# Kernel tuning notes

Hardware: AMD Instinct MI355X
Metric: run time of the kernel (lower is better)

The kernel has to match this reference:

```python
import jax, jax.numpy as jnp
import numpy as np

N_NODES = 50000
N_EDGES = 1600000
IN_FEAT = 256
HID = IN_FEAT // 2  # 128
OUT_FEAT = 256


def setup_inputs() -> dict:
    key = jax.random.key(0)
    ks = jax.random.split(key, 10)
    x = jax.random.normal(ks[0], (N_NODES, IN_FEAT), dtype=jnp.float32)
    w = jax.random.uniform(ks[1], (N_EDGES, 1), dtype=jnp.float32)
    src = jax.random.randint(ks[2], (N_EDGES,), 0, N_NODES, dtype=jnp.int32)
    dst = jax.random.randint(ks[3], (N_EDGES,), 0, N_NODES, dtype=jnp.int32)
    s = 1.0 / np.sqrt(IN_FEAT)
    W_node = jax.random.uniform(ks[4], (IN_FEAT, HID), jnp.float32, -s, s)
    b_node = jax.random.uniform(ks[5], (HID,), jnp.float32, -s, s)
    W_edge = jax.random.uniform(ks[6], (IN_FEAT, HID), jnp.float32, -s, s)
    b_edge = jax.random.uniform(ks[7], (HID,), jnp.float32, -s, s)
    s2 = 1.0 / np.sqrt(HID)
    W_mlp = jax.random.uniform(ks[8], (HID, OUT_FEAT), jnp.float32, -s2, s2)
    b_mlp = jax.random.uniform(ks[9], (OUT_FEAT,), jnp.float32, -s2, s2)
    return {"x": x, "w": w, "src": src, "dst": dst,
            "W_node": W_node, "b_node": b_node,
            "W_edge": W_edge, "b_edge": b_edge,
            "W_mlp": W_mlp, "b_mlp": b_mlp}


def reference(x, w, src, dst, W_node, b_node, W_edge, b_edge, W_mlp, b_mlp):
    # message[v] = sum_{(u->v) in E} x[u] * w_e   (src_mul_edge + sum)
    message = jax.ops.segment_sum(x[src] * w, dst, num_segments=x.shape[0])  # [N, in_feat]
    h = (x @ W_node + b_node) + (message @ W_edge + b_edge)  # [N, in_feat//2]
    # NOTE: original uses nn.LeakyReLU(True) -> negative_slope=1.0 (identity);
    # replicated faithfully.
    h = jax.nn.leaky_relu(h, negative_slope=1.0)
    return h @ W_mlp + b_mlp  # [N, out_feat]
```

## Files before the change

kernel.cpp:

```cpp
#include <hip/hip_runtime.h>


constexpr int N_NODES  = 50000;
constexpr int N_EDGES  = 1600000;
constexpr int IN_FEAT  = 256;
constexpr int HID      = 128;
constexpr int OUT_FEAT = 256;

constexpr int BIN_SZ   = 32;
constexpr int N_BINS   = (N_NODES + BIN_SZ - 1) / BIN_SZ;
constexpr int CAPBIN   = 1536;
constexpr int EPB      = 4096;
constexpr int N_CBLK   = (N_EDGES + EPB - 1) / EPB;
constexpr int GRID_M   = (N_NODES + 127) / 128;
constexpr int N_G1BLK  = GRID_M * 2;

typedef __attribute__((ext_vector_type(8))) short bf16x8;
typedef __attribute__((ext_vector_type(8))) unsigned short u16x8;
typedef __attribute__((ext_vector_type(4))) float f32x4;

static __device__ __forceinline__ unsigned short f2bf(float f) {
    unsigned u = __builtin_bit_cast(unsigned, f);
    u += 0x7FFF + ((u >> 16) & 1);
    return (unsigned short)(u >> 16);
}
static __device__ __forceinline__ float bflo(unsigned u) {
    return __builtin_bit_cast(float, u << 16);
}
static __device__ __forceinline__ float bfhi(unsigned u) {
    return __builtin_bit_cast(float, u & 0xFFFF0000u);
}

__global__ __launch_bounds__(256) void k0_convert(
    const float* __restrict__ Wn, const float* __restrict__ We,
    const float* __restrict__ Wm,
    unsigned short* __restrict__ Wcat_t, unsigned short* __restrict__ Wmt)
{
    int n = blockIdx.x;
    int k = threadIdx.x;
    float v = (n < HID) ? Wn[(size_t)k * HID + n] : We[(size_t)k * HID + (n - HID)];
    Wcat_t[(size_t)n * IN_FEAT + k] = f2bf(v);
    if (k < HID) Wmt[(size_t)n * HID + k] = f2bf(Wm[(size_t)k * OUT_FEAT + n]);
}

union SharedU {
    struct {
        int  hist[N_BINS];
        int  gbase[N_BINS];
        int  wsum[8];
        int  stot;
        int2 sorted[EPB];
    } bc;
    struct {
        unsigned short As[128][64];
        unsigned short Bs[128][64];
    } g1;
};

__global__ __launch_bounds__(512, 4) void fuse1(
    const int* __restrict__ src, const int* __restrict__ dst,
    const float* __restrict__ w, int* __restrict__ cursor,
    int2* __restrict__ entries,
    const float* __restrict__ x, const unsigned short* __restrict__ Wcat_t,
    const float* __restrict__ bn, const float* __restrict__ be,
    float* __restrict__ h0, unsigned short* __restrict__ ybf)
{
    __shared__ SharedU sh;
    const int t = threadIdx.x;
    const int wave = t >> 6, lane = t & 63;

    if (blockIdx.x < N_CBLK) {
        const int e0 = blockIdx.x * EPB;

        for (int i = t; i < N_BINS; i += 512) sh.bc.hist[i] = 0;
        __syncthreads();

        int meta[8], wb[8], rk[8], bin[8];
        #pragma unroll
        for (int k = 0; k < 8; ++k) {
            int e = e0 + t + k * 512;
            bin[k] = -1;
            if (e < N_EDGES) {
                int d = dst[e];
                int b = d >> 5;
                bin[k]  = b;
                meta[k] = src[e] | ((d & 31) << 16) | (b << 21);
                wb[k]   = __float_as_int(w[e]);
                rk[k]   = atomicAdd(&sh.bc.hist[b], 1);
            }
        }
        __syncthreads();

        const int b4 = t * 4;
        int c0 = 0, c1 = 0, c2 = 0, c3 = 0;
        if (b4 + 0 < N_BINS) c0 = sh.bc.hist[b4 + 0];
        if (b4 + 1 < N_BINS) c1 = sh.bc.hist[b4 + 1];
        if (b4 + 2 < N_BINS) c2 = sh.bc.hist[b4 + 2];
        if (b4 + 3 < N_BINS) c3 = sh.bc.hist[b4 + 3];
        const int s = c0 + c1 + c2 + c3;
        int pre = s;
        #pragma unroll
        for (int off = 1; off < 64; off <<= 1) {
            int o = __shfl_up(pre, off, 64);
            if (lane >= off) pre += o;
        }
        if (lane == 63) sh.bc.wsum[wave] = pre;
        __syncthreads();
        if (t == 0) {
            int r = 0;
            #pragma unroll
            for (int q = 0; q < 8; ++q) { int v = sh.bc.wsum[q]; sh.bc.wsum[q] = r; r += v; }
            sh.bc.stot = r;
        }
        __syncthreads();
        const int tb = sh.bc.wsum[wave] + pre - s;

        if (b4 + 0 < N_BINS) {
            sh.bc.hist[b4 + 0]  = tb;
            sh.bc.gbase[b4 + 0] = c0 ? atomicAdd(&cursor[b4 + 0], c0) : 0;
        }
        if (b4 + 1 < N_BINS) {
            sh.bc.hist[b4 + 1]  = tb + c0;
            sh.bc.gbase[b4 + 1] = c1 ? atomicAdd(&cursor[b4 + 1], c1) : 0;
        }
        if (b4 + 2 < N_BINS) {
            sh.bc.hist[b4 + 2]  = tb + c0 + c1;
            sh.bc.gbase[b4 + 2] = c2 ? atomicAdd(&cursor[b4 + 2], c2) : 0;
        }
        if (b4 + 3 < N_BINS) {
            sh.bc.hist[b4 + 3]  = tb + c0 + c1 + c2;
            sh.bc.gbase[b4 + 3] = c3 ? atomicAdd(&cursor[b4 + 3], c3) : 0;
        }
        __syncthreads();

        #pragma unroll
        for (int k = 0; k < 8; ++k)
            if (bin[k] >= 0)
                sh.bc.sorted[sh.bc.hist[bin[k]] + rk[k]] = make_int2(meta[k], wb[k]);
        __syncthreads();

        const int tot = sh.bc.stot;
        #pragma unroll
        for (int k = 0; k < 8; ++k) {
            int i = t + k * 512;
            if (i < tot) {
                int2 q = sh.bc.sorted[i];
                int b = ((unsigned)q.x) >> 21;
                int r = i - sh.bc.hist[b];
                int g = sh.bc.gbase[b] + r;
                if (g < CAPBIN)
                    entries[(size_t)b * CAPBIN + g] = make_int2(q.x & 0x1FFFFF, q.y);
            }
        }
    } else {
        const int bid2 = blockIdx.x - N_CBLK;
        const int m0 = (bid2 >> 1) * 128;
        const int nhalf = bid2 & 1;
        const int n0r = nhalf * 128;

        const int wm = wave >> 2, wn = wave & 3;
        const int la = lane & 15, kq = lane >> 4;
        const int srow = t >> 3, sc8 = t & 7;

        f32x4 acc[4][2];
        const f32x4 zero = {0.f, 0.f, 0.f, 0.f};
        #pragma unroll
        for (int i = 0; i < 4; ++i)
            #pragma unroll
            for (int j = 0; j < 2; ++j) acc[i][j] = zero;

        const float4* xg = (const float4*)x;

        for (int kt = 0; kt < 4; ++kt) {
            if (kt) __syncthreads();
            #pragma unroll
            for (int i = 0; i < 2; ++i) {
                int row = srow + i * 64;
                int node = m0 + row;
                float4 v0 = make_float4(0.f, 0.f, 0.f, 0.f), v1 = v0;
                if (node < N_NODES) {
                    v0 = xg[(size_t)node * 64 + kt * 16 + sc8 * 2];
                    v1 = xg[(size_t)node * 64 + kt * 16 + sc8 * 2 + 1];
                }
                u16x8 b;
                b[0] = f2bf(v0.x); b[1] = f2bf(v0.y); b[2] = f2bf(v0.z); b[3] = f2bf(v0.w);
                b[4] = f2bf(v1.x); b[5] = f2bf(v1.y); b[6] = f2bf(v1.z); b[7] = f2bf(v1.w);
                *(u16x8*)&sh.g1.As[row][(sc8 ^ (row & 7)) * 8] = b;
            }
            #pragma unroll
            for (int i = 0; i < 2; ++i) {
                int row = srow + i * 64;
                float4 v = *(const float4*)(
                    Wcat_t + (size_t)(n0r + row) * IN_FEAT + kt * 64 + sc8 * 8);
                *(float4*)&sh.g1.Bs[row][(sc8 ^ (row & 7)) * 8] = v;
            }
            __syncthreads();

            #pragma unroll
            for (int ks = 0; ks < 2; ++ks) {
                bf16x8 a[4], b[2];
                #pragma unroll
                for (int i = 0; i < 4; ++i) {
                    int row = wm * 64 + i * 16 + la;
                    a[i] = *(const bf16x8*)&sh.g1.As[row][((ks * 4 + kq) ^ (row & 7)) * 8];
                }
                #pragma unroll
                for (int j = 0; j < 2; ++j) {
                    int row = wn * 32 + j * 16 + la;
                    b[j] = *(const bf16x8*)&sh.g1.Bs[row][((ks * 4 + kq) ^ (row & 7)) * 8];
                }
                #pragma unroll
                for (int i = 0; i < 4; ++i)
                    #pragma unroll
                    for (int j = 0; j < 2; ++j)
                        acc[i][j] = __builtin_amdgcn_mfma_f32_16x16x32_bf16(
                            a[i], b[j], acc[i][j], 0, 0, 0);
            }
        }

        float bias[2];
        if (nhalf == 0) {
            #pragma unroll
            for (int j = 0; j < 2; ++j) {
                int n = wn * 32 + j * 16 + la;
                bias[j] = bn[n] + be[n];
            }
        }
        #pragma unroll
        for (int i = 0; i < 4; ++i) {
            int mbase = m0 + wm * 64 + i * 16 + kq * 4;
            #pragma unroll
            for (int j = 0; j < 2; ++j) {
                int n = wn * 32 + j * 16 + la;
                #pragma unroll
                for (int r = 0; r < 4; ++r) {
                    int m = mbase + r;
                    if (m < N_NODES) {
                        if (nhalf == 0)
                            h0[(size_t)m * HID + n] = acc[i][j][r] + bias[j];
                        else
                            ybf[(size_t)m * HID + n] = f2bf(acc[i][j][r]);
                    }
                }
            }
        }
    }
}

__global__ __launch_bounds__(512) void gatherB(
    const unsigned short* __restrict__ ybf, const float* __restrict__ h0,
    const int* __restrict__ cursor, const int2* __restrict__ entries,
    unsigned short* __restrict__ hbf)
{
    __shared__ int2 sorted[CAPBIN];
    __shared__ int  cnt32[BIN_SZ];
    __shared__ int  offs32[BIN_SZ];

    const int t = threadIdx.x;
    const int bin = blockIdx.x;
    const int node0 = bin * BIN_SZ;
    const int wave = t >> 6, lane = t & 63;

    const int tot = min(cursor[bin], CAPBIN);
    if (t < BIN_SZ) cnt32[t] = 0;
    __syncthreads();

    int2 held[3];
    int  hrank[3], hdloc[3];
    #pragma unroll
    for (int k = 0; k < 3; ++k) {
        hdloc[k] = -1;
        int g = t + k * 512;
        if (g < tot) {
            int2 ep = entries[(size_t)bin * CAPBIN + g];
            int dloc = ep.x >> 16;
            held[k]  = make_int2(ep.x & 0xFFFF, ep.y);
            hdloc[k] = dloc;
            hrank[k] = atomicAdd(&cnt32[dloc], 1);
        }
    }
    __syncthreads();

    if (wave == 0) {
        int v = (lane < BIN_SZ) ? cnt32[lane] : 0;
        int sum = v;
        #pragma unroll
        for (int off = 1; off < BIN_SZ; off <<= 1) {
            int o = __shfl_up(sum, off, 64);
            if (lane >= off) sum += o;
        }
        if (lane < BIN_SZ) offs32[lane] = sum - v;
    }
    __syncthreads();

    #pragma unroll
    for (int k = 0; k < 3; ++k)
        if (hdloc[k] >= 0)
            sorted[offs32[hdloc[k]] + hrank[k]] = held[k];
    __syncthreads();

    #pragma unroll
    for (int n4 = 0; n4 < 4; ++n4) {
        const int nl = wave * 4 + n4;
        const int node = node0 + nl;
        const int beg = offs32[nl];
        const int c = cnt32[nl];
        float a0 = 0.f, a1 = 0.f;
        int j = 0;
        for (; j + 4 <= c; j += 4) {
            int2 q0 = sorted[beg + j];
            int2 q1 = sorted[beg + j + 1];
            int2 q2 = sorted[beg + j + 2];
            int2 q3 = sorted[beg + j + 3];
            unsigned u0 = *(const unsigned*)&ybf[(size_t)q0.x * HID + 2 * lane];
            unsigned u1 = *(const unsigned*)&ybf[(size_t)q1.x * HID + 2 * lane];
            unsigned u2 = *(const unsigned*)&ybf[(size_t)q2.x * HID + 2 * lane];
            unsigned u3 = *(const unsigned*)&ybf[(size_t)q3.x * HID + 2 * lane];
            float w0 = __int_as_float(q0.y), w1 = __int_as_float(q1.y);
            float w2 = __int_as_float(q2.y), w3 = __int_as_float(q3.y);
            a0 += w0 * bflo(u0); a1 += w0 * bfhi(u0);
            a0 += w1 * bflo(u1); a1 += w1 * bfhi(u1);
            a0 += w2 * bflo(u2); a1 += w2 * bfhi(u2);
            a0 += w3 * bflo(u3); a1 += w3 * bfhi(u3);
        }
        for (; j < c; ++j) {
            int2 q = sorted[beg + j];
            unsigned u = *(const unsigned*)&ybf[(size_t)q.x * HID + 2 * lane];
            float wq = __int_as_float(q.y);
            a0 += wq * bflo(u); a1 += wq * bfhi(u);
        }
        if (node < N_NODES) {
            float2 hv = *(const float2*)&h0[(size_t)node * HID + 2 * lane];
            unsigned r = ((unsigned)f2bf(hv.y + a1) << 16)
                       | (unsigned)f2bf(hv.x + a0);
            *(unsigned*)&hbf[(size_t)node * HID + 2 * lane] = r;
        }
    }
}

__global__ __launch_bounds__(256, 4) void gemm2(
    const unsigned short* __restrict__ hbf, const unsigned short* __restrict__ Wmt,
    const float* __restrict__ bm, float* __restrict__ out)
{
    __shared__ unsigned short As[128][64];
    __shared__ unsigned short Bs[128][64];
    const int t = threadIdx.x;
    const int m0 = blockIdx.x * 128;
    const int n0 = blockIdx.y * 128;

    const int wave = t >> 6, lane = t & 63;
    const int wm = wave & 1, wn = wave >> 1;
    const int la = lane & 15, kq = lane >> 4;
    const int srow = t >> 3, sc8 = t & 7;

    f32x4 acc[4][4];
    const f32x4 zero = {0.f, 0.f, 0.f, 0.f};
    #pragma unroll
    for (int i = 0; i < 4; ++i)
        #pragma unroll
        for (int j = 0; j < 4; ++j) acc[i][j] = zero;

    for (int kt = 0; kt < 2; ++kt) {
        if (kt) __syncthreads();
        #pragma unroll
        for (int i = 0; i < 4; ++i) {
            int row = srow + i * 32;
            int node = m0 + row;
            if (node >= N_NODES) node = N_NODES - 1;
            float4 va = *(const float4*)(hbf + (size_t)node * HID + kt * 64 + sc8 * 8);
            float4 vb = *(const float4*)(Wmt + (size_t)(n0 + row) * HID + kt * 64 + sc8 * 8);
            *(float4*)&As[row][(sc8 ^ (row & 7)) * 8] = va;
            *(float4*)&Bs[row][(sc8 ^ (row & 7)) * 8] = vb;
        }
        __syncthreads();

        #pragma unroll
        for (int ks = 0; ks < 2; ++ks) {
            bf16x8 a[4], b[4];
            #pragma unroll
            for (int i = 0; i < 4; ++i) {
                int row = wm * 64 + i * 16 + la;
                a[i] = *(const bf16x8*)&As[row][((ks * 4 + kq) ^ (row & 7)) * 8];
            }
            #pragma unroll
            for (int j = 0; j < 4; ++j) {
                int row = wn * 64 + j * 16 + la;
                b[j] = *(const bf16x8*)&Bs[row][((ks * 4 + kq) ^ (row & 7)) * 8];
            }
            #pragma unroll
            for (int i = 0; i < 4; ++i)
                #pragma unroll
                for (int j = 0; j < 4; ++j)
                    acc[i][j] = __builtin_amdgcn_mfma_f32_16x16x32_bf16(
                        a[i], b[j], acc[i][j], 0, 0, 0);
        }
    }

    #pragma unroll
    for (int i = 0; i < 4; ++i) {
        int mbase = m0 + wm * 64 + i * 16 + kq * 4;
        #pragma unroll
        for (int j = 0; j < 4; ++j) {
            int n = n0 + wn * 64 + j * 16 + la;
            float b = bm[n];
            #pragma unroll
            for (int r = 0; r < 4; ++r) {
                int m = mbase + r;
                if (m < N_NODES)
                    out[(size_t)m * OUT_FEAT + n] = acc[i][j][r] + b;
            }
        }
    }
}

extern "C" void kernel_launch(void* const* d_in, const int* in_sizes, int n_in,
                              void* d_out, int out_size, void* d_ws, size_t ws_size,
                              hipStream_t stream) {
    const float* x   = (const float*)d_in[0];
    const float* w   = (const float*)d_in[1];
    const int*   src = (const int*)d_in[2];
    const int*   dst = (const int*)d_in[3];
    const float* Wn  = (const float*)d_in[4];
    const float* bn  = (const float*)d_in[5];
    const float* We  = (const float*)d_in[6];
    const float* be  = (const float*)d_in[7];
    const float* Wm  = (const float*)d_in[8];
    const float* bm  = (const float*)d_in[9];
    float* out = (float*)d_out;

    char* p = (char*)d_ws;
    float*          h0      = (float*)p;          p += (size_t)N_NODES * HID * 4;
    unsigned short* ybf     = (unsigned short*)p; p += (size_t)N_NODES * HID * 2;
    unsigned short* hbf     = (unsigned short*)p; p += (size_t)N_NODES * HID * 2;
    int2*           entries = (int2*)p;           p += (size_t)N_BINS * CAPBIN * 8;
    unsigned short* Wcat_t  = (unsigned short*)p; p += (size_t)256 * IN_FEAT * 2;
    unsigned short* Wmt     = (unsigned short*)p; p += (size_t)OUT_FEAT * HID * 2;
    int*            cursor  = (int*)p;            p += (size_t)N_BINS * 4;

    dim3 blk(256);

    hipMemsetAsync(cursor, 0, (size_t)N_BINS * 4, stream);
    k0_convert<<<256, blk, 0, stream>>>(Wn, We, Wm, Wcat_t, Wmt);
    fuse1<<<N_CBLK + N_G1BLK, dim3(512), 0, stream>>>(
        src, dst, w, cursor, entries, x, Wcat_t, bn, be, h0, ybf);
    gatherB<<<N_BINS, dim3(512), 0, stream>>>(ybf, h0, cursor, entries, hbf);
    gemm2<<<dim3(GRID_M, 2), blk, 0, stream>>>(hbf, Wmt, bm, out);
}
```

Baseline: 250.8 us.

## Fuse gather aggregation with output GEMM, keeping hidden tile in LDS

Merges the per-bin gather kernel and the final MLP GEMM into one kernel. Each 512-thread block processes four 32-node bins, writes the bf16 hidden rows into a swizzled LDS tile, then runs MFMA over the full 256 output columns with B fragments read directly from global memory. This removes the hbf round trip through global memory and one kernel launch. In exchange there are fewer blocks (one per 128 nodes) running the gather serially over four bins, and B is reloaded from global or cache instead of staged in LDS. The gather inner loop is also deepened to 8 outstanding loads.

```diff
diff --git a/kernel.cpp b/kernel.cpp
--- a/kernel.cpp
+++ b/kernel.cpp
@@ -247,111 +247,103 @@
     }
 }
 
-__global__ __launch_bounds__(512) void gatherB(
+__global__ __launch_bounds__(512, 4) void fuse2(
     const unsigned short* __restrict__ ybf, const float* __restrict__ h0,
     const int* __restrict__ cursor, const int2* __restrict__ entries,
-    unsigned short* __restrict__ hbf)
+    const unsigned short* __restrict__ Wmt, const float* __restrict__ bm,
+    float* __restrict__ out)
 {
+    __shared__ unsigned short As[128][128];
     __shared__ int2 sorted[CAPBIN];
     __shared__ int  cnt32[BIN_SZ];
     __shared__ int  offs32[BIN_SZ];
 
     const int t = threadIdx.x;
-    const int bin = blockIdx.x;
-    const int node0 = bin * BIN_SZ;
     const int wave = t >> 6, lane = t & 63;
-
-    const int tot = min(cursor[bin], CAPBIN);
-    if (t < BIN_SZ) cnt32[t] = 0;
-    __syncthreads();
-
-    int2 held[3];
-    int  hrank[3], hdloc[3];
-    #pragma unroll
-    for (int k = 0; k < 3; ++k) {
-        hdloc[k] = -1;
-        int g = t + k * 512;
-        if (g < tot) {
-            int2 ep = entries[(size_t)bin * CAPBIN + g];
-            int dloc = ep.x >> 16;
-            held[k]  = make_int2(ep.x & 0xFFFF, ep.y);
-            hdloc[k] = dloc;
-            hrank[k] = atomicAdd(&cnt32[dloc], 1);
-        }
+    const int m0 = blockIdx.x * 128;
+    const int bin0 = blockIdx.x * 4;
+
+    for (int sb = 0; sb < 4; ++sb) {
+        const int bin = bin0 + sb;
+        const int tot = (bin < N_BINS) ? min(cursor[bin], CAPBIN) : 0;
+        if (t < BIN_SZ) cnt32[t] = 0;
+        __syncthreads();
+
+        int2 held[3];
+        int  hrank[3], hdloc[3];
+        #pragma unroll
+        for (int k = 0; k < 3; ++k) {
+            hdloc[k] = -1;
+            int g = t + k * 512;
+            if (g < tot) {
+                int2 ep = entries[(size_t)bin * CAPBIN + g];
+                int dloc = ep.x >> 16;
+                held[k]  = make_int2(ep.x & 0xFFFF, ep.y);
+                hdloc[k] = dloc;
+                hrank[k] = atomicAdd(&cnt32[dloc], 1);
+            }
+        }
+        __syncthreads();
+
+        if (wave == 0) {
+            int v = (lane < BIN_SZ) ? cnt32[lane] : 0;
+            int sum = v;
+            #pragma unroll
+            for (int off = 1; off < BIN_SZ; off <<= 1) {
+                int o = __shfl_up(sum, off, 64);
+                if (lane >= off) sum += o;
+            }
+            if (lane < BIN_SZ) offs32[lane] = sum - v;
+        }
+        __syncthreads();
+
+        #pragma unroll
+        for (int k = 0; k < 3; ++k)
+            if (hdloc[k] >= 0)
+                sorted[offs32[hdloc[k]] + hrank[k]] = held[k];
+        __syncthreads();
+
+        #pragma unroll
+        for (int n4 = 0; n4 < 4; ++n4) {
+            const int nl = wave * 4 + n4;
+            const int row = sb * 32 + nl;
+            const int node = bin * BIN_SZ + nl;
+            const int beg = offs32[nl];
+            const int c = cnt32[nl];
+            float a0 = 0.f, a1 = 0.f;
+            int j = 0;
+            for (; j + 8 <= c; j += 8) {
+                int2 q[8]; unsigned u[8];
+                #pragma unroll
+                for (int e = 0; e < 8; ++e) q[e] = sorted[beg + j + e];
+                #pragma unroll
+                for (int e = 0; e < 8; ++e)
+                    u[e] = *(const unsigned*)&ybf[(size_t)q[e].x * HID + 2 * lane];
+                #pragma unroll
+                for (int e = 0; e < 8; ++e) {
+                    float wq = __int_as_float(q[e].y);
+                    a0 += wq * bflo(u[e]); a1 += wq * bfhi(u[e]);
+                }
+            }
+            for (; j < c; ++j) {
+                int2 q = sorted[beg + j];
+                unsigned u = *(const unsigned*)&ybf[(size_t)q.x * HID + 2 * lane];
+                float wq = __int_as_float(q.y);
+                a0 += wq * bflo(u); a1 += wq * bfhi(u);
+            }
+            float2 hv = make_float2(0.f, 0.f);
+            if (node < N_NODES)
+                hv = *(const float2*)&h0[(size_t)node * HID + 2 * lane];
+            unsigned rp = ((unsigned)f2bf(hv.y + a1) << 16)
+                        | (unsigned)f2bf(hv.x + a0);
+            int g8 = (lane >> 2) ^ (row & 7);
+            *(unsigned*)((char*)&As[row][0] + g8 * 16 + (lane & 3) * 4) = rp;
+        }
+        __syncthreads();
     }
-    __syncthreads();
-
-    if (wave == 0) {
-        int v = (lane < BIN_SZ) ? cnt32[lane] : 0;
-        int sum = v;
-        #pragma unroll
-        for (int off = 1; off < BIN_SZ; off <<= 1) {
-            int o = __shfl_up(sum, off, 64);
-            if (lane >= off) sum += o;
-        }
-        if (lane < BIN_SZ) offs32[lane] = sum - v;
-    }
-    __syncthreads();
-
-    #pragma unroll
-    for (int k = 0; k < 3; ++k)
-        if (hdloc[k] >= 0)
-            sorted[offs32[hdloc[k]] + hrank[k]] = held[k];
-    __syncthreads();
-
-    #pragma unroll
-    for (int n4 = 0; n4 < 4; ++n4) {
-        const int nl = wave * 4 + n4;
-        const int node = node0 + nl;
-        const int beg = offs32[nl];
-        const int c = cnt32[nl];
-        float a0 = 0.f, a1 = 0.f;
-        int j = 0;
-        for (; j + 4 <= c; j += 4) {
-            int2 q0 = sorted[beg + j];
-            int2 q1 = sorted[beg + j + 1];
-            int2 q2 = sorted[beg + j + 2];
-            int2 q3 = sorted[beg + j + 3];
-            unsigned u0 = *(const unsigned*)&ybf[(size_t)q0.x * HID + 2 * lane];
-            unsigned u1 = *(const unsigned*)&ybf[(size_t)q1.x * HID + 2 * lane];
-            unsigned u2 = *(const unsigned*)&ybf[(size_t)q2.x * HID + 2 * lane];
-            unsigned u3 = *(const unsigned*)&ybf[(size_t)q3.x * HID + 2 * lane];
-            float w0 = __int_as_float(q0.y), w1 = __int_as_float(q1.y);
-            float w2 = __int_as_float(q2.y), w3 = __int_as_float(q3.y);
-            a0 += w0 * bflo(u0); a1 += w0 * bfhi(u0);
-            a0 += w1 * bflo(u1); a1 += w1 * bfhi(u1);
-            a0 += w2 * bflo(u2); a1 += w2 * bfhi(u2);
-            a0 += w3 * bflo(u3); a1 += w3 * bfhi(u3);
-        }
-        for (; j < c; ++j) {
-            int2 q = sorted[beg + j];
-            unsigned u = *(const unsigned*)&ybf[(size_t)q.x * HID + 2 * lane];
-            float wq = __int_as_float(q.y);
-            a0 += wq * bflo(u); a1 += wq * bfhi(u);
-        }
-        if (node < N_NODES) {
-            float2 hv = *(const float2*)&h0[(size_t)node * HID + 2 * lane];
-            unsigned r = ((unsigned)f2bf(hv.y + a1) << 16)
-                       | (unsigned)f2bf(hv.x + a0);
-            *(unsigned*)&hbf[(size_t)node * HID + 2 * lane] = r;
-        }
-    }
-}
-
-__global__ __launch_bounds__(256, 4) void gemm2(
-    const unsigned short* __restrict__ hbf, const unsigned short* __restrict__ Wmt,
-    const float* __restrict__ bm, float* __restrict__ out)
-{
-    __shared__ unsigned short As[128][64];
-    __shared__ unsigned short Bs[128][64];
-    const int t = threadIdx.x;
-    const int m0 = blockIdx.x * 128;
-    const int n0 = blockIdx.y * 128;
-
-    const int wave = t >> 6, lane = t & 63;
-    const int wm = wave & 1, wn = wave >> 1;
+
+    const int wm = wave >> 2, wn = wave & 3;
     const int la = lane & 15, kq = lane >> 4;
-    const int srow = t >> 3, sc8 = t & 7;
 
     f32x4 acc[4][4];
     const f32x4 zero = {0.f, 0.f, 0.f, 0.f};
@@ -360,40 +352,25 @@
         #pragma unroll
         for (int j = 0; j < 4; ++j) acc[i][j] = zero;
 
-    for (int kt = 0; kt < 2; ++kt) {
-        if (kt) __syncthreads();
+    #pragma unroll
+    for (int ks = 0; ks < 4; ++ks) {
+        bf16x8 a[4], b[4];
         #pragma unroll
         for (int i = 0; i < 4; ++i) {
-            int row = srow + i * 32;
-            int node = m0 + row;
-            if (node >= N_NODES) node = N_NODES - 1;
-            float4 va = *(const float4*)(hbf + (size_t)node * HID + kt * 64 + sc8 * 8);
-            float4 vb = *(const float4*)(Wmt + (size_t)(n0 + row) * HID + kt * 64 + sc8 * 8);
-            *(float4*)&As[row][(sc8 ^ (row & 7)) * 8] = va;
-            *(float4*)&Bs[row][(sc8 ^ (row & 7)) * 8] = vb;
-        }
-        __syncthreads();
-
-        #pragma unroll
-        for (int ks = 0; ks < 2; ++ks) {
-            bf16x8 a[4], b[4];
-            #pragma unroll
-            for (int i = 0; i < 4; ++i) {
-                int row = wm * 64 + i * 16 + la;
-                a[i] = *(const bf16x8*)&As[row][((ks * 4 + kq) ^ (row & 7)) * 8];
-            }
-            #pragma unroll
-            for (int j = 0; j < 4; ++j) {
-                int row = wn * 64 + j * 16 + la;
-                b[j] = *(const bf16x8*)&Bs[row][((ks * 4 + kq) ^ (row & 7)) * 8];
-            }
-            #pragma unroll
-            for (int i = 0; i < 4; ++i)
-                #pragma unroll
-                for (int j = 0; j < 4; ++j)
-                    acc[i][j] = __builtin_amdgcn_mfma_f32_16x16x32_bf16(
-                        a[i], b[j], acc[i][j], 0, 0, 0);
-        }
+            int row = wm * 64 + i * 16 + la;
+            a[i] = *(const bf16x8*)&As[row][((ks * 4 + kq) ^ (row & 7)) * 8];
+        }
+        #pragma unroll
+        for (int j = 0; j < 4; ++j) {
+            int n = wn * 64 + j * 16 + la;
+            b[j] = *(const bf16x8*)(Wmt + (size_t)n * HID + ks * 32 + kq * 8);
+        }
+        #pragma unroll
+        for (int i = 0; i < 4; ++i)
+            #pragma unroll
+            for (int j = 0; j < 4; ++j)
+                acc[i][j] = __builtin_amdgcn_mfma_f32_16x16x32_bf16(
+                    a[i], b[j], acc[i][j], 0, 0, 0);
     }
 
     #pragma unroll
@@ -401,13 +378,13 @@
         int mbase = m0 + wm * 64 + i * 16 + kq * 4;
         #pragma unroll
         for (int j = 0; j < 4; ++j) {
-            int n = n0 + wn * 64 + j * 16 + la;
-            float b = bm[n];
+            int n = wn * 64 + j * 16 + la;
+            float bv = bm[n];
             #pragma unroll
             for (int r = 0; r < 4; ++r) {
                 int m = mbase + r;
                 if (m < N_NODES)
-                    out[(size_t)m * OUT_FEAT + n] = acc[i][j][r] + b;
+                    out[(size_t)m * OUT_FEAT + n] = acc[i][j][r] + bv;
             }
         }
     }
@@ -431,7 +408,6 @@
     char* p = (char*)d_ws;
     float*          h0      = (float*)p;          p += (size_t)N_NODES * HID * 4;
     unsigned short* ybf     = (unsigned short*)p; p += (size_t)N_NODES * HID * 2;
-    unsigned short* hbf     = (unsigned short*)p; p += (size_t)N_NODES * HID * 2;
     int2*           entries = (int2*)p;           p += (size_t)N_BINS * CAPBIN * 8;
     unsigned short* Wcat_t  = (unsigned short*)p; p += (size_t)256 * IN_FEAT * 2;
     unsigned short* Wmt     = (unsigned short*)p; p += (size_t)OUT_FEAT * HID * 2;
@@ -443,6 +419,5 @@
     k0_convert<<<256, blk, 0, stream>>>(Wn, We, Wm, Wcat_t, Wmt);
     fuse1<<<N_CBLK + N_G1BLK, dim3(512), 0, stream>>>(
         src, dst, w, cursor, entries, x, Wcat_t, bn, be, h0, ybf);
-    gatherB<<<N_BINS, dim3(512), 0, stream>>>(ybf, h0, cursor, entries, hbf);
-    gemm2<<<dim3(GRID_M, 2), blk, 0, stream>>>(hbf, Wmt, bm, out);
-}
+    fuse2<<<GRID_M, dim3(512), 0, stream>>>(ybf, h0, cursor, entries, Wmt, bm, out);
+}
```

Result: slower. 270.9 us (+8.0%).
